# Performance work log

Hardware: AMD Instinct MI355X
Metric: run time of the kernel (lower is better)

## Reference

```python
import jax, jax.numpy as jnp
import numpy as np

IN_SIZE = 5        # per-segment features: [number, In, former_number, speed0, speed1]
HIDDEN = 128
OUT_HIDDEN = 128
OUT_SIZE = 3       # input_size = output_size + 2 (structural constraint)
T_PREDICT = 4
B, T, S = 8, 128, 128


def setup_inputs() -> dict:
    key = jax.random.key(0)
    ks = jax.random.split(key, 5)
    scale = 0.05
    return {
        "input_data": jax.random.normal(ks[0], (B, T, S, IN_SIZE), jnp.float32),
        # seg_model: fused LSTM weight over concat(x, h, h_after, h_before)
        "W_cell": jax.random.normal(ks[1], (IN_SIZE + 3 * HIDDEN, 4 * HIDDEN), jnp.float32) * scale,
        "b_cell": jnp.zeros((4 * HIDDEN,), jnp.float32),
        # FCNet layerSize=[hidden, output_hidden, output]: Linear-ReLU-Linear
        "W1": jax.random.normal(ks[2], (HIDDEN, OUT_HIDDEN), jnp.float32) * scale,
        "b1": jnp.zeros((OUT_HIDDEN,), jnp.float32),
        "W2": jax.random.normal(ks[3], (OUT_HIDDEN, OUT_SIZE), jnp.float32) * scale,
        "b2": jnp.zeros((OUT_SIZE,), jnp.float32),
    }


def _cell(x, h, c, h_after, h_before, W, b):
    # LSTM cell on concat(x, h, h_after, h_before): [B,S,IN+3H] @ [IN+3H,4H]
    z = jnp.concatenate([x, h, h_after, h_before], axis=-1) @ W + b
    i, f, g, o = jnp.split(z, 4, axis=-1)
    c_new = jax.nn.sigmoid(f) * c + jax.nn.sigmoid(i) * jnp.tanh(g)
    h_new = jax.nn.sigmoid(o) * jnp.tanh(c_new)
    return h_new, c_new


def _next_input(former_input, next_input, output):
    # faithful translation of caculate_next_input
    speed_output = output[:, 1:, 1:]                    # [B,S-1,OUT-1]
    number_output = output[:, :, 0:1]                   # [B,S,1]
    speed_input = next_input[:, 0:1, 3:]                # [B,1,IN-3]
    In = jnp.concatenate([next_input[:, 0:1, 1:2], number_output[:, :-1, :]], axis=1)
    former_number = former_input[:, :, 2:3]
    number_caculate = former_number + In - number_output
    speed_next = jnp.concatenate([speed_input, speed_output], axis=1)
    return jnp.concatenate([number_output, In, number_caculate, speed_next], axis=2)


def reference(input_data, W_cell, b_cell, W1, b1, W2, b2):
    b, t, s, f = input_data.shape
    # time-major inputs for scan: x at time k and time k+1
    x_t = jnp.transpose(input_data[:, :-1], (1, 0, 2, 3))   # [T-1,B,S,F]
    x_tp1 = jnp.transpose(input_data[:, 1:], (1, 0, 2, 3))  # [T-1,B,S,F]
    h0 = jnp.zeros((b, s, HIDDEN), input_data.dtype)
    c0 = jnp.zeros((b, s, HIDDEN), input_data.dtype)

    def step(carry, xs):
        h, c = carry
        xt, xn = xs
        # spatial neighbor shift: h_after[i] = h[i+1], h_before[i] = h[i-1]
        h_after = jnp.pad(h[:, 1:, :], ((0, 0), (0, 1), (0, 0)))
        h_before = jnp.pad(h[:, :-1, :], ((0, 0), (1, 0), (0, 0)))
        h, c = _cell(xt, h, c, h_after, h_before, W_cell, b_cell)
        out = jnp.maximum(h @ W1 + b1, 0.0) @ W2 + b2
        nd = _next_input(xt, xn, out)
        return (h, c), nd

    _, nds = jax.lax.scan(step, (h0, c0), (x_t, x_tp1))     # [T-1,B,S,F]
    # original only writes outputs for time >= t_predict
    outputs = jnp.transpose(nds[T_PREDICT:], (1, 0, 2, 3))  # [B,T-TP-1,S,F]
    return outputs
```

## Files before the change

kernel.cpp:

```cpp
#include <hip/hip_runtime.h>
#include <hip/hip_bf16.h>


#define NB 8
#define NT 128
#define NS 128
#define NSTEP 127
#define TPRED 4
#define TOUT 123

typedef __attribute__((ext_vector_type(4))) float f32x4;
typedef __attribute__((ext_vector_type(8))) short s16x8;
typedef __attribute__((ext_vector_type(4))) unsigned int u32x4;

#define WS_WTC 0
#define WS_WT1 (512*384*2)
#define WS_PUB (WS_WT1 + 128*128*2)
#define WS_PUB_BYTES (2*64*2048*4)

#define BARRIER() do { \
    __builtin_amdgcn_sched_barrier(0); \
    asm volatile("s_waitcnt lgkmcnt(0)" ::: "memory"); \
    __builtin_amdgcn_s_barrier(); \
    __builtin_amdgcn_sched_barrier(0); \
} while (0)

__device__ __forceinline__ unsigned swz(unsigned off) {
    return off ^ (((off >> 8) & 7u) << 4);
}

__global__ void init_weights(const float* __restrict__ Wc, const float* __restrict__ W1,
                             __hip_bfloat16* __restrict__ WTc, __hip_bfloat16* __restrict__ WT1)
{
    int i = blockIdx.x * blockDim.x + threadIdx.x;
    if (i < 512*384) {
        int cpp = i / 384, k = i % 384;
        int n = cpp >> 6, rem = cpp & 63, g = rem >> 4, h = rem & 15;
        int oc = g*128 + 16*n + h;
        int row = (k < 128) ? (261 + k) : ((k < 256) ? (5 + (k - 128)) : (133 + (k - 256)));
        WTc[cpp*384 + k] = __float2bfloat16(Wc[row*512 + oc]);
    } else {
        int q = i - 512*384;
        if (q < 128*128) {
            int nn = q >> 7, k = q & 127;
            WT1[nn*128 + k] = __float2bfloat16(W1[k*128 + nn]);
        }
    }
}

__global__ __launch_bounds__(512, 2) void lstm_persist(
    const float* __restrict__ input, const float* __restrict__ Wc,
    const float* __restrict__ bc, const float* __restrict__ b1v,
    const float* __restrict__ W2, const float* __restrict__ b2,
    float* __restrict__ outp,
    const __hip_bfloat16* __restrict__ WTc, const __hip_bfloat16* __restrict__ WT1,
    unsigned* pub)
{
    __shared__ __align__(16) __hip_bfloat16 hl[2*130*128];
    __shared__ __align__(16) __hip_bfloat16 bl[64*136];
    __shared__ __align__(16) __hip_bfloat16 relu_l[18*128];
    __shared__ float xl[3][640];
    __shared__ float xnl[3][3];
    __shared__ float outl[17*3];
    __shared__ float w2l[3*128];
    __shared__ float b2l[3];

    const int tid  = threadIdx.x;
    const int blk  = blockIdx.x;
    const int b    = blk & 7;
    const int n    = blk >> 3;
    const int lane = tid & 63;
    const int w    = tid >> 6;
    const int arow = lane & 15;
    const int kgrp = lane >> 4;
    const int hid  = 16*n + arow;

    for (int i = tid; i < 2*130*128; i += 512) ((unsigned short*)hl)[i] = 0;
    if (tid < 384) w2l[tid] = W2[(tid & 127)*3 + (tid >> 7)];
    if (tid >= 384 && tid < 387) b2l[tid - 384] = b2[tid - 384];
    for (int i = tid; i < 64*32; i += 512) {
        int col = i >> 5, kk = i & 31;
        *(unsigned long long*)((char*)bl + col*272 + kk*8) =
            *(const unsigned long long*)((const char*)WTc + ((unsigned)(n*64 + col)*384 + 256)*2 + kk*8);
    }
    {
        const float* xp = input + (unsigned)(b*NT)*640;
        xl[0][tid] = xp[tid];
        if (tid < 128) xl[0][512 + tid] = xp[512 + tid];
        if (tid >= 509 && tid < 512) { int q = tid - 509; xnl[0][q] = xp[(q == 0) ? 1 : (q + 2)]; }
    }

    float wxr[4][5], bcr[4];
    #pragma unroll
    for (int g = 0; g < 4; ++g) {
        const int cg = g*128 + hid;
        bcr[g] = bc[cg];
        #pragma unroll
        for (int f = 0; f < 5; ++f) wxr[g][f] = Wc[f*512 + cg];
    }
    const float b1r = b1v[16*w + arow];

    s16x8 brg[4][8];
    #pragma unroll
    for (int g = 0; g < 4; ++g)
        #pragma unroll
        for (int kt = 0; kt < 8; ++kt)
            brg[g][kt] = *(const s16x8*)((const char*)WTc +
                ((unsigned)(n*64 + g*16 + arow)*384 + kt*32 + kgrp*8)*2);
    s16x8 w1r[4];
    #pragma unroll
    for (int kt = 0; kt < 4; ++kt)
        w1r[kt] = *(const s16x8*)((const char*)WT1 + ((unsigned)(16*w + arow)*128 + kt*32 + kgrp*8)*2);

    float cst[4] = {0.f, 0.f, 0.f, 0.f};
    unsigned short hregb[4] = {0, 0, 0, 0};

    __syncthreads();

    for (int j = 0; j <= NSTEP; ++j) {
        const int jm3 = j % 3;
        const unsigned hlb = (unsigned)(j & 1) * 33280u;
        if (j > 0) {
            const unsigned jt = (unsigned)j;
            const unsigned row = (unsigned)tid >> 2;
            const unsigned* pb = pub + (unsigned)((j&1)*64 + b*8)*2048 + row*16 + (tid & 3)*4;
            const int s_0 = 0 + (0 >= n), s_1 = 1 + (1 >= n), s_2 = 2 + (2 >= n), s_3 = 3 + (3 >= n),
                      s_4 = 4 + (4 >= n), s_5 = 5 + (5 >= n), s_6 = 6 + (6 >= n);
            const unsigned *q0 = pb + s_0*2048, *q1 = pb + s_1*2048, *q2 = pb + s_2*2048,
                           *q3 = pb + s_3*2048, *q4 = pb + s_4*2048, *q5 = pb + s_5*2048,
                           *q6 = pb + s_6*2048;
            u32x4 g0, g1, g2, g3, g4, g5, g6;
            for (;;) {
                asm volatile(
                    "global_load_dwordx4 %0, %7, off sc0 sc1\n\t"
                    "global_load_dwordx4 %1, %8, off sc0 sc1\n\t"
                    "global_load_dwordx4 %2, %9, off sc0 sc1\n\t"
                    "global_load_dwordx4 %3, %10, off sc0 sc1\n\t"
                    "global_load_dwordx4 %4, %11, off sc0 sc1\n\t"
                    "global_load_dwordx4 %5, %12, off sc0 sc1\n\t"
                    "global_load_dwordx4 %6, %13, off sc0 sc1\n\t"
                    "s_waitcnt vmcnt(0)"
                    : "=&v"(g0), "=&v"(g1), "=&v"(g2), "=&v"(g3), "=&v"(g4), "=&v"(g5), "=&v"(g6)
                    : "v"(q0), "v"(q1), "v"(q2), "v"(q3), "v"(q4), "v"(q5), "v"(q6)
                    : "memory");
                unsigned bad = 0;
                #define CHK(g) bad |= ((g[0]>>16)^jt) | ((g[1]>>16)^jt) | ((g[2]>>16)^jt) | ((g[3]>>16)^jt)
                CHK(g0); CHK(g1); CHK(g2); CHK(g3); CHK(g4); CHK(g5); CHK(g6);
                #undef CHK
                if (bad == 0) break;
                __builtin_amdgcn_s_sleep(2);
            }
            __builtin_amdgcn_sched_barrier(0);
            const unsigned rb = (row + 1)*256;
            const unsigned cb = (unsigned)(tid & 3)*8;
            #define PK(g) ((unsigned long long)((g[0] & 0xffffu) | (g[1] << 16)) | \
                           ((unsigned long long)((g[2] & 0xffffu) | (g[3] << 16)) << 32))
            *(unsigned long long*)((char*)hl + hlb + swz(rb + 32u*s_0 + cb)) = PK(g0);
            *(unsigned long long*)((char*)hl + hlb + swz(rb + 32u*s_1 + cb)) = PK(g1);
            *(unsigned long long*)((char*)hl + hlb + swz(rb + 32u*s_2 + cb)) = PK(g2);
            *(unsigned long long*)((char*)hl + hlb + swz(rb + 32u*s_3 + cb)) = PK(g3);
            *(unsigned long long*)((char*)hl + hlb + swz(rb + 32u*s_4 + cb)) = PK(g4);
            *(unsigned long long*)((char*)hl + hlb + swz(rb + 32u*s_5 + cb)) = PK(g5);
            *(unsigned long long*)((char*)hl + hlb + swz(rb + 32u*s_6 + cb)) = PK(g6);
            #undef PK
            #pragma unroll
            for (int r = 0; r < 4; ++r)
                *(unsigned short*)((char*)hl + hlb +
                    swz((unsigned)((16*w + kgrp*4 + r + 1)*256 + hid*2))) = hregb[r];
        }
        BARRIER();

        if (j < NSTEP) {
            f32x4 a0 = {0.f,0.f,0.f,0.f}, a1 = a0, a2 = a0, a3 = a0;
            const unsigned abase = (unsigned)((16*w + arow)*256 + kgrp*16);
            #pragma unroll
            for (int kt = 0; kt < 8; ++kt) {
                const s16x8 av = *(const s16x8*)((const char*)hl + hlb + swz(abase + kt*64));
                a0 = __builtin_amdgcn_mfma_f32_16x16x32_bf16(av, brg[0][kt], a0, 0, 0, 0);
                a1 = __builtin_amdgcn_mfma_f32_16x16x32_bf16(av, brg[1][kt], a1, 0, 0, 0);
                a2 = __builtin_amdgcn_mfma_f32_16x16x32_bf16(av, brg[2][kt], a2, 0, 0, 0);
                a3 = __builtin_amdgcn_mfma_f32_16x16x32_bf16(av, brg[3][kt], a3, 0, 0, 0);
            }
            #pragma unroll
            for (int kt = 8; kt < 12; ++kt) {
                const s16x8 av = *(const s16x8*)((const char*)hl + hlb + swz(abase + kt*64));
                const char* blb = (const char*)bl + (kt - 8)*64 + kgrp*16;
                a0 = __builtin_amdgcn_mfma_f32_16x16x32_bf16(av, *(const s16x8*)(blb + (arow      )*272), a0, 0, 0, 0);
                a1 = __builtin_amdgcn_mfma_f32_16x16x32_bf16(av, *(const s16x8*)(blb + (16 + arow )*272), a1, 0, 0, 0);
                a2 = __builtin_amdgcn_mfma_f32_16x16x32_bf16(av, *(const s16x8*)(blb + (32 + arow )*272), a2, 0, 0, 0);
                a3 = __builtin_amdgcn_mfma_f32_16x16x32_bf16(av, *(const s16x8*)(blb + (48 + arow )*272), a3, 0, 0, 0);
            }
            const unsigned jt1 = (unsigned)(j + 1);
            unsigned* pubw = pub + (unsigned)(((j+1)&1)*64 + b*8 + n)*2048;
            #pragma unroll
            for (int r = 0; r < 4; ++r) {
                const int row = 16*w + kgrp*4 + r;
                const float xv0 = xl[jm3][row*5+0], xv1 = xl[jm3][row*5+1], xv2 = xl[jm3][row*5+2],
                            xv3 = xl[jm3][row*5+3], xv4 = xl[jm3][row*5+4];
                const float iv = a0[r] + bcr[0] + xv0*wxr[0][0] + xv1*wxr[0][1] + xv2*wxr[0][2] + xv3*wxr[0][3] + xv4*wxr[0][4];
                const float fv = a1[r] + bcr[1] + xv0*wxr[1][0] + xv1*wxr[1][1] + xv2*wxr[1][2] + xv3*wxr[1][3] + xv4*wxr[1][4];
                const float gv = a2[r] + bcr[2] + xv0*wxr[2][0] + xv1*wxr[2][1] + xv2*wxr[2][2] + xv3*wxr[2][3] + xv4*wxr[2][4];
                const float ov = a3[r] + bcr[3] + xv0*wxr[3][0] + xv1*wxr[3][1] + xv2*wxr[3][2] + xv3*wxr[3][3] + xv4*wxr[3][4];
                const float si = __builtin_amdgcn_rcpf(1.f + __expf(-iv));
                const float sf = __builtin_amdgcn_rcpf(1.f + __expf(-fv));
                const float so = __builtin_amdgcn_rcpf(1.f + __expf(-ov));
                const float tg = 1.f - 2.f*__builtin_amdgcn_rcpf(__expf(2.f*gv) + 1.f);
                const float cn = sf*cst[r] + si*tg;
                cst[r] = cn;
                const float tc = 1.f - 2.f*__builtin_amdgcn_rcpf(__expf(2.f*cn) + 1.f);
                const float hn = so*tc;
                __hip_bfloat16 hbv = __float2bfloat16(hn);
                unsigned short hbits = *(unsigned short*)&hbv;
                hregb[r] = hbits;
                unsigned word = (jt1 << 16) | (unsigned)hbits;
                asm volatile("global_store_dword %0, %1, off sc0 sc1"
                             :: "v"(pubw + row*16 + arow), "v"(word) : "memory");
            }
        }

        if (j >= TPRED + 1) {
            const int jm1_3 = (j - 1) % 3;
            f32x4 c0 = {0.f,0.f,0.f,0.f}, c1 = c0;
            const unsigned w1a = (unsigned)((16*n + arow)*256 + kgrp*16);
            #pragma unroll
            for (int kt = 0; kt < 4; ++kt) {
                const s16x8 av0 = *(const s16x8*)((const char*)hl + hlb + swz(w1a + kt*64));
                const s16x8 av1 = *(const s16x8*)((const char*)hl + hlb + swz(w1a + 256 + kt*64));
                c0 = __builtin_amdgcn_mfma_f32_16x16x32_bf16(av0, w1r[kt], c0, 0, 0, 0);
                c1 = __builtin_amdgcn_mfma_f32_16x16x32_bf16(av1, w1r[kt], c1, 0, 0, 0);
            }
            #pragma unroll
            for (int r = 0; r < 4; ++r) {
                const int lr = kgrp*4 + r;
                const float v0 = fmaxf(c0[r] + b1r, 0.f);
                *(__hip_bfloat16*)((char*)relu_l + swz((unsigned)(lr*256 + (16*w + arow)*2))) = __float2bfloat16(v0);
                if (lr == 15) {
                    const float v1 = fmaxf(c1[r] + b1r, 0.f);
                    *(__hip_bfloat16*)((char*)relu_l + swz((unsigned)(16*256 + (16*w + arow)*2))) = __float2bfloat16(v1);
                }
            }
            BARRIER();
            if (tid < 51) {
                const int m = tid / 3, p = tid - m*3;
                float s = b2l[p];
                #pragma unroll
                for (int kc = 0; kc < 16; ++kc) {
                    union { s16x8 v; unsigned short u[8]; } uu;
                    uu.v = *(const s16x8*)((const char*)relu_l + swz((unsigned)(m*256 + kc*16)));
                    #pragma unroll
                    for (int e = 0; e < 8; ++e)
                        s += __uint_as_float((unsigned)uu.u[e] << 16) * w2l[p*128 + kc*8 + e];
                }
                outl[m*3 + p] = s;
            }
            if (tid < 16) {
                const int m = tid, grow = 16*n + m;
                const float no = outl[(m + 1)*3 + 0];
                float In, sp0, sp1;
                if (m == 0 && n == 0) { In = xnl[jm3][0]; sp0 = xnl[jm3][1]; sp1 = xnl[jm3][2]; }
                else { In = outl[m*3 + 0]; sp0 = outl[(m + 1)*3 + 1]; sp1 = outl[(m + 1)*3 + 2]; }
                const float former = xl[jm1_3][grow*5 + 2];
                const long base = ((long)(b*TOUT + (j - 1 - TPRED))*NS + grow)*5;
                outp[base + 0] = no;
                outp[base + 1] = In;
                outp[base + 2] = former + In - no;
                outp[base + 3] = sp0;
                outp[base + 4] = sp1;
            }
        }

        if (j < NSTEP) {
            const int jp3 = (j + 1) % 3;
            const float* xp = input + (unsigned)(b*NT + j + 1)*640;
            xl[jp3][tid] = xp[tid];
            if (tid < 128) xl[jp3][512 + tid] = xp[512 + tid];
            if (tid >= 509 && tid < 512) { int q = tid - 509; xnl[jp3][q] = xp[(q == 0) ? 1 : (q + 2)]; }
        }
    }
}

extern "C" void kernel_launch(void* const* d_in, const int* in_sizes, int n_in,
                              void* d_out, int out_size, void* d_ws, size_t ws_size,
                              hipStream_t stream) {
    const float* input = (const float*)d_in[0];
    const float* Wc    = (const float*)d_in[1];
    const float* bc    = (const float*)d_in[2];
    const float* W1    = (const float*)d_in[3];
    const float* b1    = (const float*)d_in[4];
    const float* W2    = (const float*)d_in[5];
    const float* b2    = (const float*)d_in[6];
    float* outp = (float*)d_out;
    char* ws = (char*)d_ws;

    __hip_bfloat16* WTc = (__hip_bfloat16*)(ws + WS_WTC);
    __hip_bfloat16* WT1 = (__hip_bfloat16*)(ws + WS_WT1);
    unsigned*       pub = (unsigned*)(ws + WS_PUB);

    hipMemsetAsync(ws + WS_PUB, 0, WS_PUB_BYTES, stream);
    init_weights<<<832, 256, 0, stream>>>(Wc, W1, WTc, WT1);
    lstm_persist<<<64, 512, 0, stream>>>(input, Wc, bc, b1, W2, b2, outp, WTc, WT1, pub);
}
```

Measured before the change: 952.4 us.

## Partition LSTM by segment chunk and exchange only halo rows between blocks

```diff
diff --git a/kernel.cpp b/kernel.cpp
--- a/kernel.cpp
+++ b/kernel.cpp
@@ -16,7 +16,7 @@
 #define WS_WTC 0
 #define WS_WT1 (512*384*2)
 #define WS_PUB (WS_WT1 + 128*128*2)
-#define WS_PUB_BYTES (2*64*2048*4)
+#define WS_PUB_BYTES (2*8*8*2*128*4)
 
 #define BARRIER() do { \
     __builtin_amdgcn_sched_barrier(0); \
@@ -35,20 +35,20 @@
     int i = blockIdx.x * blockDim.x + threadIdx.x;
     if (i < 512*384) {
         int cpp = i / 384, k = i % 384;
-        int n = cpp >> 6, rem = cpp & 63, g = rem >> 4, h = rem & 15;
-        int oc = g*128 + 16*n + h;
+        int q = cpp >> 6, rem = cpp & 63, g = rem >> 4, h = rem & 15;
+        int oc = g*128 + 16*q + h;
         int row = (k < 128) ? (261 + k) : ((k < 256) ? (5 + (k - 128)) : (133 + (k - 256)));
         WTc[cpp*384 + k] = __float2bfloat16(Wc[row*512 + oc]);
     } else {
-        int q = i - 512*384;
-        if (q < 128*128) {
-            int nn = q >> 7, k = q & 127;
+        int qq = i - 512*384;
+        if (qq < 128*128) {
+            int nn = qq >> 7, k = qq & 127;
             WT1[nn*128 + k] = __float2bfloat16(W1[k*128 + nn]);
         }
     }
 }
 
-__global__ __launch_bounds__(512, 2) void lstm_persist(
+__global__ __launch_bounds__(512, 1) void lstm_persist(
     const float* __restrict__ input, const float* __restrict__ Wc,
     const float* __restrict__ bc, const float* __restrict__ b1v,
     const float* __restrict__ W2, const float* __restrict__ b2,
@@ -56,11 +56,9 @@
     const __hip_bfloat16* __restrict__ WTc, const __hip_bfloat16* __restrict__ WT1,
     unsigned* pub)
 {
-    __shared__ __align__(16) __hip_bfloat16 hl[2*130*128];
-    __shared__ __align__(16) __hip_bfloat16 bl[64*136];
+    __shared__ __align__(16) __hip_bfloat16 hl[2*18*128];
     __shared__ __align__(16) __hip_bfloat16 relu_l[18*128];
-    __shared__ float xl[3][640];
-    __shared__ float xnl[3][3];
+    __shared__ float xl[3][80];
     __shared__ float outl[17*3];
     __shared__ float w2l[3*128];
     __shared__ float b2l[3];
@@ -68,135 +66,115 @@
     const int tid  = threadIdx.x;
     const int blk  = blockIdx.x;
     const int b    = blk & 7;
-    const int n    = blk >> 3;
+    const int c    = blk >> 3;
     const int lane = tid & 63;
     const int w    = tid >> 6;
     const int arow = lane & 15;
     const int kgrp = lane >> 4;
-    const int hid  = 16*n + arow;
-
-    for (int i = tid; i < 2*130*128; i += 512) ((unsigned short*)hl)[i] = 0;
+    const int hidw = 16*w + arow;
+
+    for (int i = tid; i < 2*18*128; i += 512) ((unsigned short*)hl)[i] = 0;
     if (tid < 384) w2l[tid] = W2[(tid & 127)*3 + (tid >> 7)];
     if (tid >= 384 && tid < 387) b2l[tid - 384] = b2[tid - 384];
-    for (int i = tid; i < 64*32; i += 512) {
-        int col = i >> 5, kk = i & 31;
-        *(unsigned long long*)((char*)bl + col*272 + kk*8) =
-            *(const unsigned long long*)((const char*)WTc + ((unsigned)(n*64 + col)*384 + 256)*2 + kk*8);
-    }
-    {
-        const float* xp = input + (unsigned)(b*NT)*640;
-        xl[0][tid] = xp[tid];
-        if (tid < 128) xl[0][512 + tid] = xp[512 + tid];
-        if (tid >= 509 && tid < 512) { int q = tid - 509; xnl[0][q] = xp[(q == 0) ? 1 : (q + 2)]; }
-    }
 
     float wxr[4][5], bcr[4];
     #pragma unroll
     for (int g = 0; g < 4; ++g) {
-        const int cg = g*128 + hid;
+        const int cg = g*128 + hidw;
         bcr[g] = bc[cg];
         #pragma unroll
         for (int f = 0; f < 5; ++f) wxr[g][f] = Wc[f*512 + cg];
     }
-    const float b1r = b1v[16*w + arow];
-
-    s16x8 brg[4][8];
+    const float b1r = b1v[hidw];
+
+    s16x8 brg[4][12];
     #pragma unroll
     for (int g = 0; g < 4; ++g)
         #pragma unroll
-        for (int kt = 0; kt < 8; ++kt)
+        for (int kt = 0; kt < 12; ++kt)
             brg[g][kt] = *(const s16x8*)((const char*)WTc +
-                ((unsigned)(n*64 + g*16 + arow)*384 + kt*32 + kgrp*8)*2);
+                ((unsigned)(w*64 + g*16 + arow)*384 + kt*32 + kgrp*8)*2);
     s16x8 w1r[4];
     #pragma unroll
     for (int kt = 0; kt < 4; ++kt)
-        w1r[kt] = *(const s16x8*)((const char*)WT1 + ((unsigned)(16*w + arow)*128 + kt*32 + kgrp*8)*2);
+        w1r[kt] = *(const s16x8*)((const char*)WT1 + ((unsigned)(hidw)*128 + kt*32 + kgrp*8)*2);
 
     float cst[4] = {0.f, 0.f, 0.f, 0.f};
-    unsigned short hregb[4] = {0, 0, 0, 0};
+
+    if (tid < 80) xl[0][tid] = input[((unsigned)(b*NT)*NS + 16*c)*5 + tid];
 
     __syncthreads();
 
     for (int j = 0; j <= NSTEP; ++j) {
         const int jm3 = j % 3;
-        const unsigned hlb = (unsigned)(j & 1) * 33280u;
-        if (j > 0) {
-            const unsigned jt = (unsigned)j;
-            const unsigned row = (unsigned)tid >> 2;
-            const unsigned* pb = pub + (unsigned)((j&1)*64 + b*8)*2048 + row*16 + (tid & 3)*4;
-            const int s_0 = 0 + (0 >= n), s_1 = 1 + (1 >= n), s_2 = 2 + (2 >= n), s_3 = 3 + (3 >= n),
-                      s_4 = 4 + (4 >= n), s_5 = 5 + (5 >= n), s_6 = 6 + (6 >= n);
-            const unsigned *q0 = pb + s_0*2048, *q1 = pb + s_1*2048, *q2 = pb + s_2*2048,
-                           *q3 = pb + s_3*2048, *q4 = pb + s_4*2048, *q5 = pb + s_5*2048,
-                           *q6 = pb + s_6*2048;
-            u32x4 g0, g1, g2, g3, g4, g5, g6;
-            for (;;) {
-                asm volatile(
-                    "global_load_dwordx4 %0, %7, off sc0 sc1\n\t"
-                    "global_load_dwordx4 %1, %8, off sc0 sc1\n\t"
-                    "global_load_dwordx4 %2, %9, off sc0 sc1\n\t"
-                    "global_load_dwordx4 %3, %10, off sc0 sc1\n\t"
-                    "global_load_dwordx4 %4, %11, off sc0 sc1\n\t"
-                    "global_load_dwordx4 %5, %12, off sc0 sc1\n\t"
-                    "global_load_dwordx4 %6, %13, off sc0 sc1\n\t"
-                    "s_waitcnt vmcnt(0)"
-                    : "=&v"(g0), "=&v"(g1), "=&v"(g2), "=&v"(g3), "=&v"(g4), "=&v"(g5), "=&v"(g6)
-                    : "v"(q0), "v"(q1), "v"(q2), "v"(q3), "v"(q4), "v"(q5), "v"(q6)
-                    : "memory");
-                unsigned bad = 0;
-                #define CHK(g) bad |= ((g[0]>>16)^jt) | ((g[1]>>16)^jt) | ((g[2]>>16)^jt) | ((g[3]>>16)^jt)
-                CHK(g0); CHK(g1); CHK(g2); CHK(g3); CHK(g4); CHK(g5); CHK(g6);
-                #undef CHK
-                if (bad == 0) break;
-                __builtin_amdgcn_s_sleep(2);
-            }
-            __builtin_amdgcn_sched_barrier(0);
-            const unsigned rb = (row + 1)*256;
-            const unsigned cb = (unsigned)(tid & 3)*8;
-            #define PK(g) ((unsigned long long)((g[0] & 0xffffu) | (g[1] << 16)) | \
-                           ((unsigned long long)((g[2] & 0xffffu) | (g[3] << 16)) << 32))
-            *(unsigned long long*)((char*)hl + hlb + swz(rb + 32u*s_0 + cb)) = PK(g0);
-            *(unsigned long long*)((char*)hl + hlb + swz(rb + 32u*s_1 + cb)) = PK(g1);
-            *(unsigned long long*)((char*)hl + hlb + swz(rb + 32u*s_2 + cb)) = PK(g2);
-            *(unsigned long long*)((char*)hl + hlb + swz(rb + 32u*s_3 + cb)) = PK(g3);
-            *(unsigned long long*)((char*)hl + hlb + swz(rb + 32u*s_4 + cb)) = PK(g4);
-            *(unsigned long long*)((char*)hl + hlb + swz(rb + 32u*s_5 + cb)) = PK(g5);
-            *(unsigned long long*)((char*)hl + hlb + swz(rb + 32u*s_6 + cb)) = PK(g6);
-            #undef PK
-            #pragma unroll
-            for (int r = 0; r < 4; ++r)
-                *(unsigned short*)((char*)hl + hlb +
-                    swz((unsigned)((16*w + kgrp*4 + r + 1)*256 + hid*2))) = hregb[r];
-        }
+        const unsigned hlb  = (unsigned)(j & 1) * 4608u;
+        const unsigned nhlb = (unsigned)((j + 1) & 1) * 4608u;
+
+        if (j > 0 && tid < 64) {
+            const bool left = (tid < 32);
+            if (left ? (c > 0) : (c < 7)) {
+                const unsigned jt = (unsigned)j;
+                const int nc   = left ? (c - 1) : (c + 1);
+                const int side = left ? 1 : 0;
+                const int col4 = (tid & 31) * 4;
+                const unsigned* q = pub + (unsigned)(((j & 1)*8 + b)*8 + nc)*256 + side*128 + col4;
+                u32x4 g;
+                for (;;) {
+                    asm volatile("global_load_dwordx4 %0, %1, off sc0 sc1\n\ts_waitcnt vmcnt(0)"
+                                 : "=v"(g) : "v"(q) : "memory");
+                    if ((g[0] >> 16) == jt && (g[1] >> 16) == jt &&
+                        (g[2] >> 16) == jt && (g[3] >> 16) == jt) break;
+                }
+                __builtin_amdgcn_sched_barrier(0);
+                const unsigned long long pk =
+                    (unsigned long long)(g[0] & 0xffffu)        |
+                    ((unsigned long long)(g[1] & 0xffffu) << 16) |
+                    ((unsigned long long)(g[2] & 0xffffu) << 32) |
+                    ((unsigned long long)(g[3] & 0xffffu) << 48);
+                const int row = left ? 0 : 17;
+                *(unsigned long long*)((char*)hl + hlb + swz((unsigned)(row*256 + col4*2))) = pk;
+            }
+        }
+        float xr = 0.f;
+        const bool xact = (j < NSTEP) && (tid < 80);
+        if (xact) xr = input[((unsigned)(b*NT + j + 1)*NS + 16*c)*5 + tid];
+
         BARRIER();
 
         if (j < NSTEP) {
             f32x4 a0 = {0.f,0.f,0.f,0.f}, a1 = a0, a2 = a0, a3 = a0;
-            const unsigned abase = (unsigned)((16*w + arow)*256 + kgrp*16);
-            #pragma unroll
-            for (int kt = 0; kt < 8; ++kt) {
-                const s16x8 av = *(const s16x8*)((const char*)hl + hlb + swz(abase + kt*64));
+            const unsigned ab = (unsigned)(arow*256 + kgrp*16);
+            #pragma unroll
+            for (int kt = 0; kt < 4; ++kt) {
+                const s16x8 av = *(const s16x8*)((const char*)hl + hlb + swz(ab + kt*64));
                 a0 = __builtin_amdgcn_mfma_f32_16x16x32_bf16(av, brg[0][kt], a0, 0, 0, 0);
                 a1 = __builtin_amdgcn_mfma_f32_16x16x32_bf16(av, brg[1][kt], a1, 0, 0, 0);
                 a2 = __builtin_amdgcn_mfma_f32_16x16x32_bf16(av, brg[2][kt], a2, 0, 0, 0);
                 a3 = __builtin_amdgcn_mfma_f32_16x16x32_bf16(av, brg[3][kt], a3, 0, 0, 0);
             }
             #pragma unroll
+            for (int kt = 4; kt < 8; ++kt) {
+                const s16x8 av = *(const s16x8*)((const char*)hl + hlb + swz(ab + 256 + (kt-4)*64));
+                a0 = __builtin_amdgcn_mfma_f32_16x16x32_bf16(av, brg[0][kt], a0, 0, 0, 0);
+                a1 = __builtin_amdgcn_mfma_f32_16x16x32_bf16(av, brg[1][kt], a1, 0, 0, 0);
+                a2 = __builtin_amdgcn_mfma_f32_16x16x32_bf16(av, brg[2][kt], a2, 0, 0, 0);
+                a3 = __builtin_amdgcn_mfma_f32_16x16x32_bf16(av, brg[3][kt], a3, 0, 0, 0);
+            }
+            #pragma unroll
             for (int kt = 8; kt < 12; ++kt) {
-                const s16x8 av = *(const s16x8*)((const char*)hl + hlb + swz(abase + kt*64));
-                const char* blb = (const char*)bl + (kt - 8)*64 + kgrp*16;
-                a0 = __builtin_amdgcn_mfma_f32_16x16x32_bf16(av, *(const s16x8*)(blb + (arow      )*272), a0, 0, 0, 0);
-                a1 = __builtin_amdgcn_mfma_f32_16x16x32_bf16(av, *(const s16x8*)(blb + (16 + arow )*272), a1, 0, 0, 0);
-                a2 = __builtin_amdgcn_mfma_f32_16x16x32_bf16(av, *(const s16x8*)(blb + (32 + arow )*272), a2, 0, 0, 0);
-                a3 = __builtin_amdgcn_mfma_f32_16x16x32_bf16(av, *(const s16x8*)(blb + (48 + arow )*272), a3, 0, 0, 0);
-            }
-            const unsigned jt1 = (unsigned)(j + 1);
-            unsigned* pubw = pub + (unsigned)(((j+1)&1)*64 + b*8 + n)*2048;
+                const s16x8 av = *(const s16x8*)((const char*)hl + hlb + swz(ab + 512 + (kt-8)*64));
+                a0 = __builtin_amdgcn_mfma_f32_16x16x32_bf16(av, brg[0][kt], a0, 0, 0, 0);
+                a1 = __builtin_amdgcn_mfma_f32_16x16x32_bf16(av, brg[1][kt], a1, 0, 0, 0);
+                a2 = __builtin_amdgcn_mfma_f32_16x16x32_bf16(av, brg[2][kt], a2, 0, 0, 0);
+                a3 = __builtin_amdgcn_mfma_f32_16x16x32_bf16(av, brg[3][kt], a3, 0, 0, 0);
+            }
+            asm volatile("s_waitcnt vmcnt(0)" ::: "memory");
+            unsigned short h0b = 0, h3b = 0;
             #pragma unroll
             for (int r = 0; r < 4; ++r) {
-                const int row = 16*w + kgrp*4 + r;
-                const float xv0 = xl[jm3][row*5+0], xv1 = xl[jm3][row*5+1], xv2 = xl[jm3][row*5+2],
-                            xv3 = xl[jm3][row*5+3], xv4 = xl[jm3][row*5+4];
+                const int lr0 = kgrp*4 + r;
+                const float xv0 = xl[jm3][lr0*5+0], xv1 = xl[jm3][lr0*5+1], xv2 = xl[jm3][lr0*5+2],
+                            xv3 = xl[jm3][lr0*5+3], xv4 = xl[jm3][lr0*5+4];
                 const float iv = a0[r] + bcr[0] + xv0*wxr[0][0] + xv1*wxr[0][1] + xv2*wxr[0][2] + xv3*wxr[0][3] + xv4*wxr[0][4];
                 const float fv = a1[r] + bcr[1] + xv0*wxr[1][0] + xv1*wxr[1][1] + xv2*wxr[1][2] + xv3*wxr[1][3] + xv4*wxr[1][4];
                 const float gv = a2[r] + bcr[2] + xv0*wxr[2][0] + xv1*wxr[2][1] + xv2*wxr[2][2] + xv3*wxr[2][3] + xv4*wxr[2][4];
@@ -210,18 +188,25 @@
                 const float tc = 1.f - 2.f*__builtin_amdgcn_rcpf(__expf(2.f*cn) + 1.f);
                 const float hn = so*tc;
                 __hip_bfloat16 hbv = __float2bfloat16(hn);
-                unsigned short hbits = *(unsigned short*)&hbv;
-                hregb[r] = hbits;
-                unsigned word = (jt1 << 16) | (unsigned)hbits;
+                const unsigned short hbits = *(const unsigned short*)&hbv;
+                *(unsigned short*)((char*)hl + nhlb + swz((unsigned)((lr0 + 1)*256 + hidw*2))) = hbits;
+                if (r == 0) h0b = hbits;
+                if (r == 3) h3b = hbits;
+            }
+            unsigned* pbase = pub + (unsigned)((((j+1) & 1)*8 + b)*8 + c)*256;
+            const unsigned jt1 = (unsigned)(j + 1) << 16;
+            if (c > 0 && kgrp == 0)
                 asm volatile("global_store_dword %0, %1, off sc0 sc1"
-                             :: "v"(pubw + row*16 + arow), "v"(word) : "memory");
-            }
+                             :: "v"(pbase + hidw), "v"(jt1 | (unsigned)h0b) : "memory");
+            if (c < 7 && kgrp == 3)
+                asm volatile("global_store_dword %0, %1, off sc0 sc1"
+                             :: "v"(pbase + 128 + hidw), "v"(jt1 | (unsigned)h3b) : "memory");
         }
 
         if (j >= TPRED + 1) {
             const int jm1_3 = (j - 1) % 3;
             f32x4 c0 = {0.f,0.f,0.f,0.f}, c1 = c0;
-            const unsigned w1a = (unsigned)((16*n + arow)*256 + kgrp*16);
+            const unsigned w1a = (unsigned)(arow*256 + kgrp*16);
             #pragma unroll
             for (int kt = 0; kt < 4; ++kt) {
                 const s16x8 av0 = *(const s16x8*)((const char*)hl + hlb + swz(w1a + kt*64));
@@ -233,10 +218,10 @@
             for (int r = 0; r < 4; ++r) {
                 const int lr = kgrp*4 + r;
                 const float v0 = fmaxf(c0[r] + b1r, 0.f);
-                *(__hip_bfloat16*)((char*)relu_l + swz((unsigned)(lr*256 + (16*w + arow)*2))) = __float2bfloat16(v0);
+                *(__hip_bfloat16*)((char*)relu_l + swz((unsigned)(lr*256 + hidw*2))) = __float2bfloat16(v0);
                 if (lr == 15) {
                     const float v1 = fmaxf(c1[r] + b1r, 0.f);
-                    *(__hip_bfloat16*)((char*)relu_l + swz((unsigned)(16*256 + (16*w + arow)*2))) = __float2bfloat16(v1);
+                    *(__hip_bfloat16*)((char*)relu_l + swz((unsigned)(16*256 + hidw*2))) = __float2bfloat16(v1);
                 }
             }
             BARRIER();
@@ -254,12 +239,12 @@
                 outl[m*3 + p] = s;
             }
             if (tid < 16) {
-                const int m = tid, grow = 16*n + m;
+                const int m = tid, grow = 16*c + m;
                 const float no = outl[(m + 1)*3 + 0];
                 float In, sp0, sp1;
-                if (m == 0 && n == 0) { In = xnl[jm3][0]; sp0 = xnl[jm3][1]; sp1 = xnl[jm3][2]; }
+                if (m == 0 && c == 0) { In = xl[jm3][1]; sp0 = xl[jm3][3]; sp1 = xl[jm3][4]; }
                 else { In = outl[m*3 + 0]; sp0 = outl[(m + 1)*3 + 1]; sp1 = outl[(m + 1)*3 + 2]; }
-                const float former = xl[jm1_3][grow*5 + 2];
+                const float former = xl[jm1_3][m*5 + 2];
                 const long base = ((long)(b*TOUT + (j - 1 - TPRED))*NS + grow)*5;
                 outp[base + 0] = no;
                 outp[base + 1] = In;
@@ -269,13 +254,7 @@
             }
         }
 
-        if (j < NSTEP) {
-            const int jp3 = (j + 1) % 3;
-            const float* xp = input + (unsigned)(b*NT + j + 1)*640;
-            xl[jp3][tid] = xp[tid];
-            if (tid < 128) xl[jp3][512 + tid] = xp[512 + tid];
-            if (tid >= 509 && tid < 512) { int q = tid - 509; xnl[jp3][q] = xp[(q == 0) ? 1 : (q + 2)]; }
-        }
+        if (xact) xl[(j + 1) % 3][tid] = xr;
     }
 }
 
```

Result: slower. 1.003 ms (+5.3%).
